# Performance work log

Measured on AMD Instinct MI355X. Metric: run time of the kernel, lower is better.

Reference implementation:

```python
import jax, jax.numpy as jnp
import numpy as np

B, T = 2048, 8192


def setup_inputs() -> dict:
    key = jax.random.key(0)
    k1, k2 = jax.random.split(key)
    x = jax.random.normal(k1, (B, T, 1), dtype=jnp.float32)
    out_prev0 = jnp.zeros((B, 1, 1), dtype=jnp.float32)
    # weights = [m_lo, m_up, c_lo, c_up]; keep slopes positive for well-conditioned division in h()
    weights = jax.random.uniform(k2, (4,), dtype=jnp.float32, minval=0.5, maxval=1.5)
    return {"x": x, "out_prev0": out_prev0, "weights": weights}


def reference(x, out_prev0, weights):
    # x: [B, T, 1], out_prev0: [B, 1, 1], weights: [4]
    m_lo, m_up, c_lo, c_up = weights[0], weights[1], weights[2], weights[3]
    # h(s) = 1 if s <= 0 else 0; since all elements of h's output are overwritten by
    # masked assignment in the torch code, it carries zero gradient (same as a hard step).
    m_lo_d = jax.lax.stop_gradient(m_lo)  # mirrors .detach() inside the step-fn args
    m_up_d = jax.lax.stop_gradient(m_up)
    c_lo_d = jax.lax.stop_gradient(c_lo)
    c_up_d = jax.lax.stop_gradient(c_up)

    def step(prev, xt):
        # prev, xt: [B, 1]
        s1 = (m_lo_d * xt + m_lo_d * c_lo_d - prev) / m_lo_d
        s2 = (prev - m_up_d * xt - m_up_d * c_up_d) / m_up_d
        f1 = (s1 <= 0).astype(xt.dtype)
        f2 = (s2 <= 0).astype(xt.dtype)
        out = (m_lo * xt * f1 + m_lo * c_lo * f1
               + m_up * xt * f2 + m_up * c_up * f2
               + prev * (1.0 - f1) * (1.0 - f2))
        return out, out

    xs = jnp.transpose(x, (1, 0, 2))          # [T, B, 1]
    prev0 = out_prev0[:, 0, :]                # [B, 1]
    _, ys = jax.lax.scan(step, prev0, xs)     # ys: [T, B, 1]
    custom_output = jnp.transpose(ys, (1, 0, 2))  # [B, T, 1]
    return custom_output
```

## Files before the change

### kernel.cpp

```cpp
#include <hip/hip_runtime.h>
#include <stdint.h>


namespace {

constexpr int kB  = 2048;
constexpr int kT  = 8192;
constexpr int kNC = 128;
constexpr int kRPB = 2;
constexpr int kGrid = kB / kRPB;

__device__ __forceinline__ float bstep(float xv, float prev, float m_lo, float m_up,
                                       float mlc, float muc) {
  float A1 = __fmul_rn(m_lo, xv);
  float B1 = __fadd_rn(A1, mlc);
  float A2 = __fmul_rn(m_up, xv);
  float B2 = __fadd_rn(A2, muc);
  float C  = __fadd_rn(__fadd_rn(B1, A2), muc);
  float u  = __fsub_rn(prev, A2);
  bool  f1 = (B1 <= prev);
  bool  f2 = (u <= muc);
  float hi = f2 ? C  : B1;
  float lo = f2 ? B2 : prev;
  return f1 ? hi : lo;
}

__device__ __forceinline__ void issue_row(const float* __restrict__ xrow,
                                          float4* __restrict__ buf, int tid) {
#pragma unroll
  for (int j = 0; j < 16; ++j) {
    const int s  = j * 128 + tid;
    const int cc = s >> 4, fs = s & 15;
    const int g  = cc * 16 + (fs ^ (cc & 15));
    __builtin_amdgcn_global_load_lds(
        (const __attribute__((address_space(1))) uint32_t*)(xrow + 4 * (size_t)g),
        (__attribute__((address_space(3))) uint32_t*)(buf + s),
        16, 0, 0);
  }
}

template <bool kLast>
__device__ __forceinline__ void process_row(
    const float* __restrict__ x,
    float4* __restrict__ sb, float* __restrict__ se0, float* __restrict__ se1,
    int* __restrict__ sflag, float* __restrict__ sfix,
    float* __restrict__ out, int r, int c, float p0r,
    float m_lo, float m_up, float mlc, float muc) {
  float pa = (c == 0) ? p0r : 0.0f;
#pragma unroll
  for (int q = 0; q < 16; ++q) {
    const float4 xv = sb[c * 16 + (q ^ (c & 15))];
    pa = bstep(xv.x, pa, m_lo, m_up, mlc, muc);
    pa = bstep(xv.y, pa, m_lo, m_up, mlc, muc);
    pa = bstep(xv.z, pa, m_lo, m_up, mlc, muc);
    pa = bstep(xv.w, pa, m_lo, m_up, mlc, muc);
  }
  se0[c] = pa;
  __syncthreads();

  float pb = (c == 0) ? p0r : se0[c - 1];
#pragma unroll
  for (int q = 0; q < 16; ++q) {
    const int slot = c * 16 + (q ^ (c & 15));
    const float4 xv = sb[slot];
    float o0 = bstep(xv.x, pb, m_lo, m_up, mlc, muc);
    float o1 = bstep(xv.y, o0, m_lo, m_up, mlc, muc);
    float o2 = bstep(xv.z, o1, m_lo, m_up, mlc, muc);
    float o3 = bstep(xv.w, o2, m_lo, m_up, mlc, muc);
    sb[slot] = make_float4(o0, o1, o2, o3);
    pb = o3;
  }
  se1[c] = pb;

  const bool conv = (c == kNC - 1) || (pa == pb);
  const unsigned long long bal = __ballot(conv);
  if ((c & 63) == 0) sflag[c >> 6] = (bal == ~0ull);
  __syncthreads();

  if (!(sflag[0] && sflag[1])) {
    float t = se1[0];
    for (int cc = 1; cc < kNC; ++cc) {
      const bool valid = (se0[cc - 1] == t);
      if (valid) {
        t = se1[cc];
      } else {
        __syncthreads();
        if (c == cc) {
          const float4* xg =
              reinterpret_cast<const float4*>(x + (size_t)r * kT + cc * 64);
          float pf = t;
#pragma unroll
          for (int q = 0; q < 16; ++q) {
            const float4 xv = xg[q];
            float o0 = bstep(xv.x, pf, m_lo, m_up, mlc, muc);
            float o1 = bstep(xv.y, o0, m_lo, m_up, mlc, muc);
            float o2 = bstep(xv.z, o1, m_lo, m_up, mlc, muc);
            float o3 = bstep(xv.w, o2, m_lo, m_up, mlc, muc);
            sb[c * 16 + (q ^ (c & 15))] = make_float4(o0, o1, o2, o3);
            pf = o3;
          }
          *sfix = pf;
        }
        __syncthreads();
        t = *sfix;
      }
    }
    __syncthreads();
  }

  float4* o4 = reinterpret_cast<float4*>(out + (size_t)r * kT);
#pragma unroll
  for (int j = 0; j < 16; ++j) {
    const int g  = j * 128 + c;
    const int cc = g >> 4, f = g & 15;
    o4[g] = sb[cc * 16 + (f ^ (cc & 15))];
  }
  if (!kLast) {
    __syncthreads();
  }
}

__global__ __launch_bounds__(128, 2) void backlash_fused(
    const float* __restrict__ x, const float* __restrict__ p0,
    const float* __restrict__ w, float* __restrict__ out) {
  __shared__ float4 sb[kNC * 16];
  __shared__ float  se0[kNC], se1[kNC];
  __shared__ int    sflag[2];
  __shared__ float  sfix;

  const int c  = threadIdx.x;
  const int r0 = blockIdx.x * kRPB;
  const float m_lo = w[0], m_up = w[1];
  const float mlc = __fmul_rn(m_lo, w[2]), muc = __fmul_rn(m_up, w[3]);

  issue_row(x + (size_t)r0 * kT, sb, c);
  __syncthreads();
  process_row<false>(x, sb, se0, se1, sflag, &sfix, out, r0, c, p0[r0],
                     m_lo, m_up, mlc, muc);

  issue_row(x + (size_t)(r0 + 1) * kT, sb, c);
  __syncthreads();
  process_row<true>(x, sb, se0, se1, sflag, &sfix, out, r0 + 1, c, p0[r0 + 1],
                    m_lo, m_up, mlc, muc);
}

}

extern "C" void kernel_launch(void* const* d_in, const int* in_sizes, int n_in,
                              void* d_out, int out_size, void* d_ws, size_t ws_size,
                              hipStream_t stream) {
  const float* x  = (const float*)d_in[0];
  const float* p0 = (const float*)d_in[1];
  const float* w  = (const float*)d_in[2];
  float* out = (float*)d_out;
  (void)in_sizes; (void)n_in; (void)out_size; (void)d_ws; (void)ws_size;

  backlash_fused<<<kGrid, kNC, 0, stream>>>(x, p0, w, out);
}
```

Measured before the change: 132.6 us.

## Process each row with a single wavefront over register-double-buffered segments

Replaces the 128-thread, two-rows-per-block scheme with one 64-lane wavefront per row. The row is processed as four 2048-element segments, with the carry passed between segments. Cross-chunk carries move through wave shuffles and ballot instead of shared memory and __syncthreads. The next segment is prefetched into registers while the current one is processed, which drops block-level barriers but leaves each row handled more serially across segments. The grid grows to 2048 single-wave blocks, and the repair path for non-converged chunks now runs at segment granularity.

Result: faster. 115.5 us (-12.9%).

```diff
diff --git a/kernel.cpp b/kernel.cpp
--- a/kernel.cpp
+++ b/kernel.cpp
@@ -4,11 +4,10 @@
 
 namespace {
 
-constexpr int kB  = 2048;
-constexpr int kT  = 8192;
-constexpr int kNC = 128;
-constexpr int kRPB = 2;
-constexpr int kGrid = kB / kRPB;
+constexpr int kT    = 8192;
+constexpr int kSeg  = 2048;
+constexpr int kF4   = kSeg / 4;
+constexpr int kNSeg = kT / kSeg;
 
 __device__ __forceinline__ float bstep(float xv, float prev, float m_lo, float m_up,
                                        float mlc, float muc) {
@@ -25,43 +24,41 @@
   return f1 ? hi : lo;
 }
 
-__device__ __forceinline__ void issue_row(const float* __restrict__ xrow,
-                                          float4* __restrict__ buf, int tid) {
+__device__ __forceinline__ void seg_fetch(const float4* __restrict__ xr, int seg,
+                                          int l, float4 (&buf)[8]) {
 #pragma unroll
-  for (int j = 0; j < 16; ++j) {
-    const int s  = j * 128 + tid;
-    const int cc = s >> 4, fs = s & 15;
-    const int g  = cc * 16 + (fs ^ (cc & 15));
-    __builtin_amdgcn_global_load_lds(
-        (const __attribute__((address_space(1))) uint32_t*)(xrow + 4 * (size_t)g),
-        (__attribute__((address_space(3))) uint32_t*)(buf + s),
-        16, 0, 0);
+  for (int j = 0; j < 8; ++j) buf[j] = xr[seg * kF4 + j * 64 + l];
+}
+
+__device__ __forceinline__ void seg_stage(float4* __restrict__ sb, int l,
+                                          const float4 (&buf)[8]) {
+#pragma unroll
+  for (int j = 0; j < 8; ++j) {
+    const int g = j * 64 + l, c = g >> 3, f = g & 7;
+    sb[c * 8 + (f ^ (c & 7))] = buf[j];
   }
 }
 
-template <bool kLast>
-__device__ __forceinline__ void process_row(
-    const float* __restrict__ x,
-    float4* __restrict__ sb, float* __restrict__ se0, float* __restrict__ se1,
-    int* __restrict__ sflag, float* __restrict__ sfix,
-    float* __restrict__ out, int r, int c, float p0r,
+__device__ __forceinline__ float process_seg(
+    float4* __restrict__ sb, const float* __restrict__ x,
+    float4* __restrict__ o4, int r, int seg, int l, float t,
     float m_lo, float m_up, float mlc, float muc) {
-  float pa = (c == 0) ? p0r : 0.0f;
+  float pa = (l == 0) ? t : 0.0f;
 #pragma unroll
-  for (int q = 0; q < 16; ++q) {
-    const float4 xv = sb[c * 16 + (q ^ (c & 15))];
+  for (int f = 0; f < 8; ++f) {
+    const float4 xv = sb[l * 8 + (f ^ (l & 7))];
     pa = bstep(xv.x, pa, m_lo, m_up, mlc, muc);
     pa = bstep(xv.y, pa, m_lo, m_up, mlc, muc);
     pa = bstep(xv.z, pa, m_lo, m_up, mlc, muc);
     pa = bstep(xv.w, pa, m_lo, m_up, mlc, muc);
   }
-  se0[c] = pa;
-  __syncthreads();
 
-  float pb = (c == 0) ? p0r : se0[c - 1];
+  float ent = __shfl_up(pa, 1);
+  if (l == 0) ent = t;
+  float pb = ent;
 #pragma unroll
-  for (int q = 0; q < 16; ++q) {
-    const int slot = c * 16 + (q ^ (c & 15));
+  for (int f = 0; f < 8; ++f) {
+    const int slot = l * 8 + (f ^ (l & 7));
     const float4 xv = sb[slot];
     float o0 = bstep(xv.x, pb, m_lo, m_up, mlc, muc);
     float o1 = bstep(xv.y, o0, m_lo, m_up, mlc, muc);
@@ -70,78 +67,76 @@
     sb[slot] = make_float4(o0, o1, o2, o3);
     pb = o3;
   }
-  se1[c] = pb;
 
-  const bool conv = (c == kNC - 1) || (pa == pb);
-  const unsigned long long bal = __ballot(conv);
-  if ((c & 63) == 0) sflag[c >> 6] = (bal == ~0ull);
-  __syncthreads();
-
-  if (!(sflag[0] && sflag[1])) {
-    float t = se1[0];
-    for (int cc = 1; cc < kNC; ++cc) {
-      const bool valid = (se0[cc - 1] == t);
-      if (valid) {
-        t = se1[cc];
+  const bool conv = (pa == pb) || (l == 63);
+  if (__ballot(conv) == ~0ull) {
+    t = __shfl(pb, 63);
+  } else {
+    float tc = __shfl(pb, 0);
+    for (int cc = 1; cc < 64; ++cc) {
+      const float used = __shfl(pa, cc - 1);
+      if (used == tc) {
+        tc = __shfl(pb, cc);
       } else {
-        __syncthreads();
-        if (c == cc) {
-          const float4* xg =
-              reinterpret_cast<const float4*>(x + (size_t)r * kT + cc * 64);
-          float pf = t;
+        float pf = tc;
+        if (l == cc) {
+          const float4* xg = reinterpret_cast<const float4*>(
+              x + (size_t)r * kT + seg * kSeg + cc * 32);
 #pragma unroll
-          for (int q = 0; q < 16; ++q) {
-            const float4 xv = xg[q];
+          for (int f = 0; f < 8; ++f) {
+            const float4 xv = xg[f];
             float o0 = bstep(xv.x, pf, m_lo, m_up, mlc, muc);
             float o1 = bstep(xv.y, o0, m_lo, m_up, mlc, muc);
             float o2 = bstep(xv.z, o1, m_lo, m_up, mlc, muc);
             float o3 = bstep(xv.w, o2, m_lo, m_up, mlc, muc);
-            sb[c * 16 + (q ^ (c & 15))] = make_float4(o0, o1, o2, o3);
+            sb[l * 8 + (f ^ (l & 7))] = make_float4(o0, o1, o2, o3);
             pf = o3;
           }
-          *sfix = pf;
         }
-        __syncthreads();
-        t = *sfix;
+        tc = __shfl(pf, cc);
       }
     }
-    __syncthreads();
+    t = tc;
   }
 
-  float4* o4 = reinterpret_cast<float4*>(out + (size_t)r * kT);
 #pragma unroll
-  for (int j = 0; j < 16; ++j) {
-    const int g  = j * 128 + c;
-    const int cc = g >> 4, f = g & 15;
-    o4[g] = sb[cc * 16 + (f ^ (cc & 15))];
+  for (int j = 0; j < 8; ++j) {
+    const int g = j * 64 + l, c = g >> 3, f = g & 7;
+    o4[seg * kF4 + g] = sb[c * 8 + (f ^ (c & 7))];
   }
-  if (!kLast) {
-    __syncthreads();
-  }
+  return t;
 }
 
-__global__ __launch_bounds__(128, 2) void backlash_fused(
+__global__ __launch_bounds__(64, 2) void backlash_wave(
     const float* __restrict__ x, const float* __restrict__ p0,
     const float* __restrict__ w, float* __restrict__ out) {
-  __shared__ float4 sb[kNC * 16];
-  __shared__ float  se0[kNC], se1[kNC];
-  __shared__ int    sflag[2];
-  __shared__ float  sfix;
+  __shared__ float4 sb[kF4];
 
-  const int c  = threadIdx.x;
-  const int r0 = blockIdx.x * kRPB;
+  const int l = threadIdx.x;
+  const int r = blockIdx.x;
   const float m_lo = w[0], m_up = w[1];
   const float mlc = __fmul_rn(m_lo, w[2]), muc = __fmul_rn(m_up, w[3]);
+  const float4* xr = reinterpret_cast<const float4*>(x + (size_t)r * kT);
+  float4* o4 = reinterpret_cast<float4*>(out + (size_t)r * kT);
 
-  issue_row(x + (size_t)r0 * kT, sb, c);
-  __syncthreads();
-  process_row<false>(x, sb, se0, se1, sflag, &sfix, out, r0, c, p0[r0],
-                     m_lo, m_up, mlc, muc);
+  float t = p0[r];
+  float4 A[8], B[8];
 
-  issue_row(x + (size_t)(r0 + 1) * kT, sb, c);
-  __syncthreads();
-  process_row<true>(x, sb, se0, se1, sflag, &sfix, out, r0 + 1, c, p0[r0 + 1],
-                    m_lo, m_up, mlc, muc);
+  seg_fetch(xr, 0, l, A);
+  seg_stage(sb, l, A);
+  seg_fetch(xr, 1, l, B);
+  t = process_seg(sb, x, o4, r, 0, l, t, m_lo, m_up, mlc, muc);
+
+  seg_stage(sb, l, B);
+  seg_fetch(xr, 2, l, A);
+  t = process_seg(sb, x, o4, r, 1, l, t, m_lo, m_up, mlc, muc);
+
+  seg_stage(sb, l, A);
+  seg_fetch(xr, 3, l, B);
+  t = process_seg(sb, x, o4, r, 2, l, t, m_lo, m_up, mlc, muc);
+
+  seg_stage(sb, l, B);
+  t = process_seg(sb, x, o4, r, 3, l, t, m_lo, m_up, mlc, muc);
 }
 
 }
@@ -155,5 +150,5 @@
   float* out = (float*)d_out;
   (void)in_sizes; (void)n_in; (void)out_size; (void)d_ws; (void)ws_size;
 
-  backlash_fused<<<kGrid, kNC, 0, stream>>>(x, p0, w, out);
+  backlash_wave<<<2048, 64, 0, stream>>>(x, p0, w, out);
 }
```
